# Kernel tuning notes

Measured on AMD Instinct MI355X. Metric: run time of the kernel, lower is better.

## Reference

```python
import jax, jax.numpy as jnp
import numpy as np
from jax import lax

B, T, H = 2, 1024, 2048
NH, D = 8, 128          # heads, head_dim
P = NH * D              # projection size
K = 4                   # short conv kernel size
EPS = 1e-6
SCALE = D ** -0.5


def _causal_conv_silu(x, w):
    # x: (B,T,C); w: (C,K) depthwise causal conv followed by silu (ShortConvolution)
    C = w.shape[0]
    kern = jnp.transpose(w)[:, None, :]  # (K,1,C)
    y = lax.conv_general_dilated(x, kern, window_strides=(1,), padding=[(K - 1, 0)],
                                 dimension_numbers=('NWC', 'WIO', 'NWC'),
                                 feature_group_count=C)
    return jax.nn.silu(y)


def _l2norm(x):
    return x * jax.lax.rsqrt(jnp.sum(x * x, axis=-1, keepdims=True) + EPS)


def _forward(hidden_states, Wq, Wk, Wv, conv_q, conv_k, conv_v, A_log, dt_bias,
             Wfa, Wfb, Wb, Wga, Wgb, norm_weight, Wo):
    x = hidden_states                                # (B,T,H)
    q = _causal_conv_silu(x @ Wq.T, conv_q)          # (B,T,P)
    k = _causal_conv_silu(x @ Wk.T, conv_k)
    v = _causal_conv_silu(x @ Wv.T, conv_v)
    # fused_kda_gate: g = -exp(A_log) * softplus(f_b(f_a(x)) + dt_bias), per (h,d) channel
    gf = (x @ Wfa.T) @ Wfb.T                         # (B,T,P) low-rank gate proj
    gf = gf.reshape(B, T, NH, D) + dt_bias.reshape(NH, D)
    g = -jnp.exp(A_log)[None, None, :, None] * jax.nn.softplus(gf)  # (B,T,NH,D) log-decay <= 0
    beta = jax.nn.sigmoid(x @ Wb.T)                  # (B,T,NH)
    q = _l2norm(q.reshape(B, T, NH, D)) * SCALE      # use_qk_l2norm_in_kernel + 1/sqrt(d) scale
    k = _l2norm(k.reshape(B, T, NH, D))
    v = v.reshape(B, T, NH, D)

    # gated delta-rule recurrence (KDA): per-key-channel decay, beta-weighted delta update
    def step(S, inp):
        q_t, k_t, v_t, g_t, b_t = inp                # (B,NH,D), beta (B,NH)
        S = S * jnp.exp(g_t)[..., None]              # decay rows (key dim) of S[.,.,dk,dv]
        kv = jnp.einsum('bhk,bhkv->bhv', k_t, S)
        delta = (v_t - kv) * b_t[..., None]
        S = S + jnp.einsum('bhk,bhv->bhkv', k_t, delta)
        o_t = jnp.einsum('bhk,bhkv->bhv', q_t, S)
        return S, o_t

    tfirst = lambda a: jnp.moveaxis(a, 1, 0)         # time-major for scan
    S0 = jnp.zeros((B, NH, D, D), x.dtype)
    _, o = lax.scan(step, S0, (tfirst(q), tfirst(k), tfirst(v), tfirst(g), tfirst(beta)))
    o = jnp.moveaxis(o, 0, 1)                        # (B,T,NH,D)

    # FusedRMSNormGated(sigmoid): gate applied before RMS normalization (Mamba2 convention)
    gate = ((x @ Wga.T) @ Wgb.T).reshape(B, T, NH, D)
    og = o * jax.nn.sigmoid(gate)
    og = og * jax.lax.rsqrt(jnp.mean(og * og, axis=-1, keepdims=True) + EPS) * norm_weight
    return og.reshape(B * T, P) @ Wo.T               # (B*T, H)


def setup_inputs():
    ks = jax.random.split(jax.random.key(0), 16)
    s = 0.02
    f32 = jnp.float32
    return {
        'hidden_states': jax.random.normal(ks[0], (B, T, H), f32),
        'Wq': jax.random.normal(ks[1], (P, H), f32) * s,
        'Wk': jax.random.normal(ks[2], (P, H), f32) * s,
        'Wv': jax.random.normal(ks[3], (P, H), f32) * s,
        'conv_q': jax.random.normal(ks[4], (P, K), f32) * 0.3,
        'conv_k': jax.random.normal(ks[5], (P, K), f32) * 0.3,
        'conv_v': jax.random.normal(ks[6], (P, K), f32) * 0.3,
        'A_log': jnp.log(jax.random.uniform(ks[7], (NH,), f32, 1.0, 16.0)),
        'dt_bias': jax.random.normal(ks[8], (P,), f32) * 0.5,
        'Wfa': jax.random.normal(ks[9], (D, H), f32) * s,
        'Wfb': jax.random.normal(ks[10], (P, D), f32) * s,
        'Wb': jax.random.normal(ks[11], (NH, H), f32) * s,
        'Wga': jax.random.normal(ks[12], (D, H), f32) * s,
        'Wgb': jax.random.normal(ks[13], (P, D), f32) * s,
        'norm_weight': jnp.ones((D,), f32),
        'Wo': jax.random.normal(ks[14], (H, P), f32) * s,
    }


def reference(hidden_states, Wq, Wk, Wv, conv_q, conv_k, conv_v, A_log, dt_bias,
              Wfa, Wfb, Wb, Wga, Wgb, norm_weight, Wo):
    return _forward(hidden_states, Wq, Wk, Wv, conv_q, conv_k, conv_v, A_log, dt_bias,
                    Wfa, Wfb, Wb, Wga, Wgb, norm_weight, Wo)
```

## Files before the change

kernel.cpp:

```cpp
#include <hip/hip_runtime.h>
#include <hip/hip_bf16.h>
#include <cstddef>
#include <cstdint>

#define Bb 2
#define Tt 1024
#define Hh 2048
#define NHh 8
#define Dd 128
#define Pp (NHh * Dd)
#define Kk 4
#define EPSf 1e-6f
#define SCALEf 0.08838834764831845f
#define DVQ 16
#define CHUNK 8

typedef short bf16x8 __attribute__((ext_vector_type(8)));
typedef float f32x4 __attribute__((ext_vector_type(4)));

template <int CTRL>
__device__ __forceinline__ float dpp_add(float x) {
  int yi = __builtin_amdgcn_update_dpp(0, __builtin_bit_cast(int, x), CTRL, 0xF, 0xF, true);
  return x + __builtin_bit_cast(float, yi);
}
__device__ __forceinline__ float row16_sum(float x) {
  x = dpp_add<0xB1>(x);
  x = dpp_add<0x4E>(x);
  x = dpp_add<0x124>(x);
  x = dpp_add<0x128>(x);
  return x;
}

__device__ __forceinline__ void gload_lds16(const void* g, void* l) {
  __builtin_amdgcn_global_load_lds((const __attribute__((address_space(1))) void*)g,
                                   (__attribute__((address_space(3))) void*)l, 16, 0, 0);
}

__global__ __launch_bounds__(256) void cvt_bf16(const float* __restrict__ src,
                                                __hip_bfloat16* __restrict__ dst, int n) {
  const int i = (blockIdx.x * 256 + threadIdx.x) * 8;
  if (i >= n) return;
  const float4 a = *reinterpret_cast<const float4*>(src + i);
  const float4 b = *reinterpret_cast<const float4*>(src + i + 4);
  __hip_bfloat16 t[8];
  t[0] = __float2bfloat16(a.x); t[1] = __float2bfloat16(a.y);
  t[2] = __float2bfloat16(a.z); t[3] = __float2bfloat16(a.w);
  t[4] = __float2bfloat16(b.x); t[5] = __float2bfloat16(b.y);
  t[6] = __float2bfloat16(b.z); t[7] = __float2bfloat16(b.w);
  *reinterpret_cast<uint4*>(dst + i) = *reinterpret_cast<const uint4*>(t);
}

__global__ __launch_bounds__(256) void cvt_bf16_x4(const float* __restrict__ s0,
                                                   const float* __restrict__ s1,
                                                   const float* __restrict__ s2,
                                                   const float* __restrict__ s3,
                                                   __hip_bfloat16* __restrict__ d0,
                                                   __hip_bfloat16* __restrict__ d1,
                                                   __hip_bfloat16* __restrict__ d2,
                                                   __hip_bfloat16* __restrict__ d3,
                                                   int nper) {
  const int bpa = nper / 2048;
  const int a = blockIdx.x / bpa;
  const int i = (blockIdx.x % bpa) * 2048 + threadIdx.x * 8;
  const float* src = (a == 0) ? s0 : (a == 1) ? s1 : (a == 2) ? s2 : s3;
  __hip_bfloat16* dst = (a == 0) ? d0 : (a == 1) ? d1 : (a == 2) ? d2 : d3;
  const float4 x = *reinterpret_cast<const float4*>(src + i);
  const float4 y = *reinterpret_cast<const float4*>(src + i + 4);
  __hip_bfloat16 t[8];
  t[0] = __float2bfloat16(x.x); t[1] = __float2bfloat16(x.y);
  t[2] = __float2bfloat16(x.z); t[3] = __float2bfloat16(x.w);
  t[4] = __float2bfloat16(y.x); t[5] = __float2bfloat16(y.y);
  t[6] = __float2bfloat16(y.z); t[7] = __float2bfloat16(y.w);
  *reinterpret_cast<uint4*>(dst + i) = *reinterpret_cast<const uint4*>(t);
}

__global__ __launch_bounds__(256) void cvt_split(const float* __restrict__ src,
                                                 __hip_bfloat16* __restrict__ hi,
                                                 __hip_bfloat16* __restrict__ lo, int n) {
  const int i = (blockIdx.x * 256 + threadIdx.x) * 8;
  if (i >= n) return;
  __hip_bfloat16 th[8], tl[8];
#pragma unroll
  for (int j = 0; j < 2; j++) {
    const float4 a = *reinterpret_cast<const float4*>(src + i + j * 4);
    const float f[4] = {a.x, a.y, a.z, a.w};
#pragma unroll
    for (int e = 0; e < 4; e++) {
      const __hip_bfloat16 h = __float2bfloat16(f[e]);
      th[j * 4 + e] = h;
      tl[j * 4 + e] = __float2bfloat16(f[e] - __bfloat162float(h));
    }
  }
  *reinterpret_cast<uint4*>(hi + i) = *reinterpret_cast<const uint4*>(th);
  *reinterpret_cast<uint4*>(lo + i) = *reinterpret_cast<const uint4*>(tl);
}

__global__ __launch_bounds__(256) void transpose_f32(const float* __restrict__ src,
                                                     float* __restrict__ dst, int R, int C) {
  __shared__ float t[32][33];
  const int bx = blockIdx.x * 32, by = blockIdx.y * 32;
  const int tx = threadIdx.x & 31, ty = threadIdx.x >> 5;
#pragma unroll
  for (int i = ty; i < 32; i += 8) {
    const int r = by + i, c = bx + tx;
    if (r < R && c < C) t[i][tx] = src[(size_t)r * C + c];
  }
  __syncthreads();
#pragma unroll
  for (int i = ty; i < 32; i += 8) {
    const int c = bx + i, r = by + tx;
    if (c < C && r < R) dst[(size_t)c * R + r] = t[tx][i];
  }
}

__global__ __launch_bounds__(256) void gemm_bf16_lds(const __hip_bfloat16* __restrict__ A,
                                                     const __hip_bfloat16* __restrict__ B,
                                                     float* __restrict__ C,
                                                     __hip_bfloat16* __restrict__ Cbf,
                                                     int M, int N, int K, int outmode) {
  __shared__ __align__(16) __hip_bfloat16 As[128 * 64];
  __shared__ __align__(16) __hip_bfloat16 Bs[128 * 64];
  const int tid = threadIdx.x;
  const int wave = tid >> 6;
  const int lane = tid & 63;
  const int wm = (wave >> 1) * 64;
  const int wn = (wave & 1) * 64;
  const int bm = blockIdx.y * 128;
  const int bn = blockIdx.x * 128;
  const int l15 = lane & 15;
  const int l4 = lane >> 4;
  const int srow = lane >> 3;
  const int scol = (lane & 7) * 8;

  f32x4 acc[4][4];
#pragma unroll
  for (int i = 0; i < 4; i++)
#pragma unroll
    for (int j = 0; j < 4; j++) acc[i][j] = (f32x4){0.f, 0.f, 0.f, 0.f};

  for (int k0 = 0; k0 < K; k0 += 64) {
#pragma unroll
    for (int i = 0; i < 4; i++) {
      const int s = wave * 4 + i;
      const int row = s * 8 + srow;
      gload_lds16(A + (size_t)(bm + row) * K + k0 + scol, &As[s * 512]);
      gload_lds16(B + (size_t)(bn + row) * K + k0 + scol, &Bs[s * 512]);
    }
    __syncthreads();
    bf16x8 af[4][2], bfv[4][2];
#pragma unroll
    for (int kf = 0; kf < 2; kf++) {
      const int kc = kf * 32 + l4 * 8;
#pragma unroll
      for (int mf = 0; mf < 4; mf++)
        af[mf][kf] = *reinterpret_cast<const bf16x8*>(&As[(wm + mf * 16 + l15) * 64 + kc]);
#pragma unroll
      for (int nf = 0; nf < 4; nf++)
        bfv[nf][kf] = *reinterpret_cast<const bf16x8*>(&Bs[(wn + nf * 16 + l15) * 64 + kc]);
    }
#pragma unroll
    for (int kf = 0; kf < 2; kf++)
#pragma unroll
      for (int mf = 0; mf < 4; mf++)
#pragma unroll
        for (int nf = 0; nf < 4; nf++)
          acc[mf][nf] = __builtin_amdgcn_mfma_f32_16x16x32_bf16(af[mf][kf], bfv[nf][kf],
                                                                acc[mf][nf], 0, 0, 0);
    __syncthreads();
  }
#pragma unroll
  for (int mf = 0; mf < 4; mf++) {
#pragma unroll
    for (int nf = 0; nf < 4; nf++) {
      const int col = bn + wn + nf * 16 + l15;
#pragma unroll
      for (int r = 0; r < 4; r++) {
        const int row = bm + wm + mf * 16 + l4 * 4 + r;
        if (outmode == 0) C[(size_t)row * N + col] = acc[mf][nf][r];
        else Cbf[(size_t)row * N + col] = __float2bfloat16(acc[mf][nf][r]);
      }
    }
  }
}

__global__ __launch_bounds__(256) void gemm_bf16_3t_lds(const __hip_bfloat16* __restrict__ Ahi,
                                                        const __hip_bfloat16* __restrict__ Alo,
                                                        const __hip_bfloat16* __restrict__ Bhi,
                                                        const __hip_bfloat16* __restrict__ Blo,
                                                        float* __restrict__ C,
                                                        int M, int N, int K) {
  __shared__ __align__(16) __hip_bfloat16 Ahs[64 * 64];
  __shared__ __align__(16) __hip_bfloat16 Als[64 * 64];
  __shared__ __align__(16) __hip_bfloat16 Bhs[128 * 64];
  __shared__ __align__(16) __hip_bfloat16 Bls[128 * 64];
  const int tid = threadIdx.x;
  const int wave = tid >> 6;
  const int lane = tid & 63;
  const int wm = (wave >> 1) * 32;
  const int wn = (wave & 1) * 64;
  const int bm = blockIdx.y * 64;
  const int bn = blockIdx.x * 128;
  const int l15 = lane & 15;
  const int l4 = lane >> 4;
  const int srow = lane >> 3;
  const int scol = (lane & 7) * 8;

  f32x4 acc[2][4];
#pragma unroll
  for (int i = 0; i < 2; i++)
#pragma unroll
    for (int j = 0; j < 4; j++) acc[i][j] = (f32x4){0.f, 0.f, 0.f, 0.f};

  for (int k0 = 0; k0 < K; k0 += 64) {
#pragma unroll
    for (int i = 0; i < 12; i++) {
      const int sid = wave * 12 + i;
      if (sid < 8) {
        const int row = sid * 8 + srow;
        gload_lds16(Ahi + (size_t)(bm + row) * K + k0 + scol, &Ahs[sid * 512]);
      } else if (sid < 16) {
        const int row = (sid - 8) * 8 + srow;
        gload_lds16(Alo + (size_t)(bm + row) * K + k0 + scol, &Als[(sid - 8) * 512]);
      } else if (sid < 32) {
        const int row = (sid - 16) * 8 + srow;
        gload_lds16(Bhi + (size_t)(bn + row) * K + k0 + scol, &Bhs[(sid - 16) * 512]);
      } else {
        const int row = (sid - 32) * 8 + srow;
        gload_lds16(Blo + (size_t)(bn + row) * K + k0 + scol, &Bls[(sid - 32) * 512]);
      }
    }
    __syncthreads();
#pragma unroll
    for (int kf = 0; kf < 2; kf++) {
      const int kc = kf * 32 + l4 * 8;
      bf16x8 ah[2], al[2], bh[4], bl[4];
#pragma unroll
      for (int mf = 0; mf < 2; mf++) {
        ah[mf] = *reinterpret_cast<const bf16x8*>(&Ahs[(wm + mf * 16 + l15) * 64 + kc]);
        al[mf] = *reinterpret_cast<const bf16x8*>(&Als[(wm + mf * 16 + l15) * 64 + kc]);
      }
#pragma unroll
      for (int nf = 0; nf < 4; nf++) {
        bh[nf] = *reinterpret_cast<const bf16x8*>(&Bhs[(wn + nf * 16 + l15) * 64 + kc]);
        bl[nf] = *reinterpret_cast<const bf16x8*>(&Bls[(wn + nf * 16 + l15) * 64 + kc]);
      }
#pragma unroll
      for (int mf = 0; mf < 2; mf++)
#pragma unroll
        for (int nf = 0; nf < 4; nf++) {
          acc[mf][nf] = __builtin_amdgcn_mfma_f32_16x16x32_bf16(ah[mf], bh[nf], acc[mf][nf], 0, 0, 0);
          acc[mf][nf] = __builtin_amdgcn_mfma_f32_16x16x32_bf16(ah[mf], bl[nf], acc[mf][nf], 0, 0, 0);
          acc[mf][nf] = __builtin_amdgcn_mfma_f32_16x16x32_bf16(al[mf], bh[nf], acc[mf][nf], 0, 0, 0);
        }
    }
    __syncthreads();
  }
#pragma unroll
  for (int mf = 0; mf < 2; mf++)
#pragma unroll
    for (int nf = 0; nf < 4; nf++) {
      const int col = bn + wn + nf * 16 + l15;
#pragma unroll
      for (int r = 0; r < 4; r++) {
        const int row = bm + wm + mf * 16 + l4 * 4 + r;
        C[(size_t)row * N + col] = acc[mf][nf][r];
      }
    }
}

__global__ __launch_bounds__(256) void gemm_nt(const float* __restrict__ A,
                                               const float* __restrict__ Bm,
                                               float* __restrict__ C,
                                               int M, int N, int Kd) {
  __shared__ float As[16][64];
  __shared__ float Bs[16][64];
  const int bm = blockIdx.y * 64;
  const int bn = blockIdx.x * 64;
  const int tid = threadIdx.x;
  const int tx = tid & 15;
  const int ty = tid >> 4;
  const int lr = tid >> 2;
  const int lc = (tid & 3) << 2;
  float acc[4][4];
#pragma unroll
  for (int i = 0; i < 4; i++)
#pragma unroll
    for (int j = 0; j < 4; j++) acc[i][j] = 0.f;
  for (int k0 = 0; k0 < Kd; k0 += 16) {
    float4 a4 = make_float4(0.f, 0.f, 0.f, 0.f);
    float4 b4 = make_float4(0.f, 0.f, 0.f, 0.f);
    const int ar = bm + lr;
    if (ar < M) a4 = *reinterpret_cast<const float4*>(A + (size_t)ar * Kd + k0 + lc);
    const int br = bn + lr;
    if (br < N) b4 = *reinterpret_cast<const float4*>(Bm + (size_t)br * Kd + k0 + lc);
    As[lc + 0][lr] = a4.x; As[lc + 1][lr] = a4.y; As[lc + 2][lr] = a4.z; As[lc + 3][lr] = a4.w;
    Bs[lc + 0][lr] = b4.x; Bs[lc + 1][lr] = b4.y; Bs[lc + 2][lr] = b4.z; Bs[lc + 3][lr] = b4.w;
    __syncthreads();
#pragma unroll
    for (int kk = 0; kk < 16; kk++) {
      float4 av = *reinterpret_cast<const float4*>(&As[kk][ty << 2]);
      float4 bv = *reinterpret_cast<const float4*>(&Bs[kk][tx << 2]);
      float a[4] = {av.x, av.y, av.z, av.w};
      float b[4] = {bv.x, bv.y, bv.z, bv.w};
#pragma unroll
      for (int i = 0; i < 4; i++)
#pragma unroll
        for (int j = 0; j < 4; j++) acc[i][j] += a[i] * b[j];
    }
    __syncthreads();
  }
#pragma unroll
  for (int i = 0; i < 4; i++) {
    const int row = bm + (ty << 2) + i;
    if (row >= M) continue;
#pragma unroll
    for (int j = 0; j < 4; j++) {
      const int col = bn + (tx << 2) + j;
      if (col < N) C[(size_t)row * N + col] = acc[i][j];
    }
  }
}

__global__ __launch_bounds__(256) void beta_kernel(const float* __restrict__ x,
                                                   const float* __restrict__ Wb,
                                                   float* __restrict__ beta) {
  __shared__ float xs[Hh];
  const int m = blockIdx.x;
  const int tid = threadIdx.x;
  for (int i = tid; i < Hh; i += 256) xs[i] = x[(size_t)m * Hh + i];
  __syncthreads();
  const int h = tid >> 5;
  const int lane = tid & 31;
  float acc = 0.f;
  for (int i = lane; i < Hh; i += 32) acc += xs[i] * Wb[(size_t)h * Hh + i];
#pragma unroll
  for (int o = 16; o > 0; o >>= 1) acc += __shfl_down(acc, o, 32);
  if (lane == 0) beta[(size_t)m * NHh + h] = 1.f / (1.f + expf(-acc));
}

__global__ __launch_bounds__(256) void g_kernel(float* __restrict__ gbuf,
                                                const float* __restrict__ dtb,
                                                const float* __restrict__ A_log) {
  const size_t i = (size_t)blockIdx.x * 256 + threadIdx.x;
  const int c = (int)(i % Pp);
  const int h = c / Dd;
  const float xv = gbuf[i] + dtb[c];
  const float sp = (xv > 20.f) ? xv : log1pf(expf(xv));
  gbuf[i] = expf(-expf(A_log[h]) * sp);
}

__global__ __launch_bounds__(128) void conv_silu_norm(const float* __restrict__ xin,
                                                      const float* __restrict__ w,
                                                      float* __restrict__ out,
                                                      int mode, int instride, int coff) {
  const int idx = blockIdx.x;
  const int h = idx % NHh;
  const int bt = idx / NHh;
  const int t = bt % Tt;
  const int d = threadIdx.x;
  const int c = h * Dd + d;
  float acc = 0.f;
#pragma unroll
  for (int j = 0; j < Kk; j++) {
    const int tt = t - (Kk - 1) + j;
    float xv = 0.f;
    if (tt >= 0) xv = xin[(size_t)(bt - (Kk - 1) + j) * instride + coff + c];
    acc += w[c * Kk + j] * xv;
  }
  float y = acc / (1.f + expf(-acc));
  float r = y;
  if (mode > 0) {
    float ss = y * y;
#pragma unroll
    for (int o = 32; o > 0; o >>= 1) ss += __shfl_down(ss, o);
    __shared__ float red[2];
    if ((d & 63) == 0) red[d >> 6] = ss;
    __syncthreads();
    const float tot = red[0] + red[1];
    const float inv = rsqrtf(tot + EPSf);
    r = y * inv * (mode == 2 ? SCALEf : 1.f);
  }
  out[(size_t)bt * Pp + c] = r;
}

__global__ __launch_bounds__(128) void scan_kernel(const float* __restrict__ q,
                                                   const float* __restrict__ k,
                                                   const float* __restrict__ v,
                                                   const float* __restrict__ eg,
                                                   const float* __restrict__ beta,
                                                   float* __restrict__ o) {
  const int blk = blockIdx.x;
  const int bh = blk & 15;
  const int dvq = blk >> 4;
  const int b = bh >> 3, h = bh & 7;
  const int tid = threadIdx.x;
  const int qr = tid & 15;
  const int dvl = tid >> 4;
  const int dv = dvq * 8 + dvl;

  __shared__ __align__(16) float qs[2][CHUNK][16][12];
  __shared__ __align__(16) float ks[2][CHUNK][16][12];
  __shared__ __align__(16) float legs[2][CHUNK][16][12];
  __shared__ float vs[2][CHUNK][8];
  __shared__ float betas[2][CHUNK];

  float s[8];
#pragma unroll
  for (int i = 0; i < 8; i++) s[i] = 0.f;

  const size_t base = (size_t)(b * Tt) * Pp + h * Dd;
  const int le = tid;

  float rq[CHUNK], rk[CHUNK], re[CHUNK], rv[CHUNK], rb = 0.f;
  auto load_chunk = [&](int t0) {
    const size_t coff = base + (size_t)t0 * Pp;
#pragma unroll
    for (int j = 0; j < CHUNK; j++) {
      rq[j] = q[coff + (size_t)j * Pp + le];
      rk[j] = k[coff + (size_t)j * Pp + le];
      re[j] = eg[coff + (size_t)j * Pp + le];
    }
    if (tid < 8) {
#pragma unroll
      for (int j = 0; j < CHUNK; j++) rv[j] = v[coff + (size_t)j * Pp + dvq * 8 + tid];
    } else if (tid < 8 + CHUNK) {
      rb = beta[(size_t)(b * Tt + t0 + tid - 8) * NHh + h];
    }
  };
  auto write_lds = [&](int bufw) {
#pragma unroll
    for (int j = 0; j < CHUNK; j++) {
      qs[bufw][j][le >> 3][le & 7] = rq[j];
      ks[bufw][j][le >> 3][le & 7] = rk[j];
      legs[bufw][j][le >> 3][le & 7] = re[j];
    }
    if (tid < 8) {
#pragma unroll
      for (int j = 0; j < CHUNK; j++) vs[bufw][j][tid] = rv[j];
    } else if (tid < 8 + CHUNK) {
      betas[bufw][tid - 8] = rb;
    }
  };

  load_chunk(0);
  write_lds(0);
  __syncthreads();
  const int NC = Tt / CHUNK;
  size_t off = base;
  for (int c = 0; c < NC; c++) {
    if (c + 1 < NC) load_chunk((c + 1) * CHUNK);
    const int buf = c & 1;
    float vv[CHUNK], bb[CHUNK], opart[CHUNK];
#pragma unroll
    for (int j = 0; j < CHUNK; j++) { vv[j] = vs[buf][j][dvl]; bb[j] = betas[buf][j]; }

    float4 ck0 = *reinterpret_cast<const float4*>(&ks[buf][0][qr][0]);
    float4 ck1 = *reinterpret_cast<const float4*>(&ks[buf][0][qr][4]);
    float4 ce0 = *reinterpret_cast<const float4*>(&legs[buf][0][qr][0]);
    float4 ce1 = *reinterpret_cast<const float4*>(&legs[buf][0][qr][4]);
    float4 cq0 = *reinterpret_cast<const float4*>(&qs[buf][0][qr][0]);
    float4 cq1 = *reinterpret_cast<const float4*>(&qs[buf][0][qr][4]);
    float kt0 = ck0.x * ce0.x, kt1 = ck0.y * ce0.y, kt2 = ck0.z * ce0.z, kt3 = ck0.w * ce0.w;
    float kt4 = ck1.x * ce1.x, kt5 = ck1.y * ce1.y, kt6 = ck1.z * ce1.z, kt7 = ck1.w * ce1.w;

#pragma unroll
    for (int j = 0; j < CHUNK; j++) {
      float4 nk0, nk1, ne0, ne1, nq0, nq1;
      if (j + 1 < CHUNK) {
        nk0 = *reinterpret_cast<const float4*>(&ks[buf][j + 1][qr][0]);
        nk1 = *reinterpret_cast<const float4*>(&ks[buf][j + 1][qr][4]);
        ne0 = *reinterpret_cast<const float4*>(&legs[buf][j + 1][qr][0]);
        ne1 = *reinterpret_cast<const float4*>(&legs[buf][j + 1][qr][4]);
        nq0 = *reinterpret_cast<const float4*>(&qs[buf][j + 1][qr][0]);
        nq1 = *reinterpret_cast<const float4*>(&qs[buf][j + 1][qr][4]);
      }
      const float es0 = ce0.x * s[0], es1 = ce0.y * s[1], es2 = ce0.z * s[2], es3 = ce0.w * s[3];
      const float es4 = ce1.x * s[4], es5 = ce1.y * s[5], es6 = ce1.z * s[6], es7 = ce1.w * s[7];
      float kva = kt0 * s[0] + kt4 * s[4];
      float kvb = kt1 * s[1] + kt5 * s[5];
      float kvc = kt2 * s[2] + kt6 * s[6];
      float kvd = kt3 * s[3] + kt7 * s[7];
      const float kvp = row16_sum((kva + kvb) + (kvc + kvd));
      const float delta = (vv[j] - kvp) * bb[j];
      s[0] = fmaf(ck0.x, delta, es0); float oa = cq0.x * s[0];
      s[1] = fmaf(ck0.y, delta, es1); float ob = cq0.y * s[1];
      s[2] = fmaf(ck0.z, delta, es2); float oc = cq0.z * s[2];
      s[3] = fmaf(ck0.w, delta, es3); float od = cq0.w * s[3];
      s[4] = fmaf(ck1.x, delta, es4); oa += cq1.x * s[4];
      s[5] = fmaf(ck1.y, delta, es5); ob += cq1.y * s[5];
      s[6] = fmaf(ck1.z, delta, es6); oc += cq1.z * s[6];
      s[7] = fmaf(ck1.w, delta, es7); od += cq1.w * s[7];
      opart[j] = (oa + ob) + (oc + od);
      if (j + 1 < CHUNK) {
        ck0 = nk0; ck1 = nk1; ce0 = ne0; ce1 = ne1; cq0 = nq0; cq1 = nq1;
        kt0 = ck0.x * ce0.x; kt1 = ck0.y * ce0.y; kt2 = ck0.z * ce0.z; kt3 = ck0.w * ce0.w;
        kt4 = ck1.x * ce1.x; kt5 = ck1.y * ce1.y; kt6 = ck1.z * ce1.z; kt7 = ck1.w * ce1.w;
      }
    }
#pragma unroll
    for (int j = 0; j < CHUNK; j++) opart[j] = row16_sum(opart[j]);
    if (qr == 0) {
#pragma unroll
      for (int j = 0; j < CHUNK; j++) o[off + (size_t)j * Pp + dv] = opart[j];
    }
    if (c + 1 < NC) write_lds(buf ^ 1);
    __syncthreads();
    off += (size_t)CHUNK * Pp;
  }
}

__global__ __launch_bounds__(128) void gated_norm(float* __restrict__ o,
                                                  const float* __restrict__ gate,
                                                  int gstride,
                                                  const float* __restrict__ nw,
                                                  __hip_bfloat16* __restrict__ ogbf) {
  const int idx = blockIdx.x;
  const int h = idx % NHh;
  const int bt = idx / NHh;
  const int d = threadIdx.x;
  const size_t off = (size_t)bt * Pp + h * Dd;
  const float ov = o[off + d];
  const float gt = gate[(size_t)bt * gstride + h * Dd + d];
  const float val = ov / (1.f + expf(-gt));
  float ss = val * val;
#pragma unroll
  for (int sh = 32; sh > 0; sh >>= 1) ss += __shfl_down(ss, sh);
  __shared__ float red[2];
  if ((d & 63) == 0) red[d >> 6] = ss;
  __syncthreads();
  const float mean = (red[0] + red[1]) * (1.f / Dd);
  const float res = val * rsqrtf(mean + EPSf) * nw[d];
  if (ogbf != nullptr) ogbf[off + d] = __float2bfloat16(res);
  else o[off + d] = res;
}

extern "C" void kernel_launch(void* const* d_in, const int* in_sizes, int n_in,
                              void* d_out, int out_size, void* d_ws, size_t ws_size,
                              hipStream_t stream) {
  const float* x     = (const float*)d_in[0];
  const float* Wq    = (const float*)d_in[1];
  const float* Wk    = (const float*)d_in[2];
  const float* Wv    = (const float*)d_in[3];
  const float* cq    = (const float*)d_in[4];
  const float* ck    = (const float*)d_in[5];
  const float* cv    = (const float*)d_in[6];
  const float* A_log = (const float*)d_in[7];
  const float* dtb   = (const float*)d_in[8];
  const float* Wfa   = (const float*)d_in[9];
  const float* Wfb   = (const float*)d_in[10];
  const float* Wb    = (const float*)d_in[11];
  const float* Wga   = (const float*)d_in[12];
  const float* Wgb   = (const float*)d_in[13];
  const float* nw    = (const float*)d_in[14];
  const float* Wo    = (const float*)d_in[15];
  float* outp = (float*)d_out;

  const int M = Bb * Tt;
  const size_t MP = (size_t)M * Pp;
  float* ws = (float*)d_ws;
  float* qkvpre = ws;
  float* qb   = qkvpre + 4 * MP;
  float* kb   = qb + MP;
  float* vb   = kb + MP;
  float* gbuf = vb + MP;
  float* obuf = gbuf + MP;
  float* betab = obuf + MP;
  float* WfaT = betab + (size_t)M * NHh;
  float* WgaT = WfaT + (size_t)Hh * Dd;
  float* f32end = WgaT + (size_t)Hh * Dd;
  float* Wcombf = obuf;

  __hip_bfloat16* xhi    = (__hip_bfloat16*)f32end;
  __hip_bfloat16* xlo    = xhi + (size_t)M * Hh;
  __hip_bfloat16* Wqkvbf = xlo + (size_t)M * Hh;
  __hip_bfloat16* Wobf   = Wqkvbf + (size_t)4 * Pp * Hh;
  __hip_bfloat16* WfaThi = Wobf + (size_t)Hh * Pp;
  __hip_bfloat16* WfaTlo = WfaThi + (size_t)Hh * Dd;
  __hip_bfloat16* Wfbhi  = WfaTlo + (size_t)Hh * Dd;
  __hip_bfloat16* Wfblo  = Wfbhi + (size_t)Pp * Dd;
  __hip_bfloat16* WgaTbf = Wfblo + (size_t)Pp * Dd;
  __hip_bfloat16* Wgbbf  = WgaTbf + (size_t)Hh * Dd;
  __hip_bfloat16* Wcombhi = Wgbbf + (size_t)Pp * Dd;
  __hip_bfloat16* Wcomblo = Wcombhi + (size_t)Pp * Hh;
  __hip_bfloat16* end = Wcomblo + (size_t)Pp * Hh;
  __hip_bfloat16* ogbf = xlo;
  const bool use_mfma = ws_size >= (size_t)((char*)end - (char*)d_ws);

  const dim3 blk(256);
  if (use_mfma) {
    cvt_split<<<(int)((size_t)M * Hh / 2048), blk, 0, stream>>>(x, xhi, xlo, M * Hh);
    cvt_bf16_x4<<<4 * (int)((size_t)Pp * Hh / 2048), blk, 0, stream>>>(
        Wq, Wk, Wv, Wo, Wqkvbf, Wqkvbf + (size_t)Pp * Hh, Wqkvbf + (size_t)2 * Pp * Hh,
        Wobf, Pp * Hh);
    transpose_f32<<<dim3(Hh / 32, Dd / 32), blk, 0, stream>>>(Wfa, WfaT, Dd, Hh);
    transpose_f32<<<dim3(Hh / 32, Dd / 32), blk, 0, stream>>>(Wga, WgaT, Dd, Hh);
    cvt_split<<<(int)((size_t)Hh * Dd / 2048), blk, 0, stream>>>(WfaT, WfaThi, WfaTlo, Hh * Dd);
    cvt_split<<<(int)((size_t)Pp * Dd / 2048), blk, 0, stream>>>(Wfb, Wfbhi, Wfblo, Pp * Dd);
    cvt_bf16<<<(int)((size_t)Hh * Dd / 2048), blk, 0, stream>>>(WgaT, WgaTbf, Hh * Dd);
    cvt_bf16<<<(int)((size_t)Pp * Dd / 2048), blk, 0, stream>>>(Wgb, Wgbbf, Pp * Dd);
    gemm_bf16_3t_lds<<<dim3(Hh / 128, Pp / 64), blk, 0, stream>>>(Wfbhi, Wfblo, WfaThi, WfaTlo,
                                                                  Wcombf, Pp, Hh, Dd);
    gemm_bf16_lds<<<dim3(Hh / 128, Pp / 128), blk, 0, stream>>>(Wgbbf, WgaTbf, nullptr,
                                                                Wqkvbf + (size_t)3 * Pp * Hh,
                                                                Pp, Hh, Dd, 1);
    cvt_split<<<(int)((size_t)Pp * Hh / 2048), blk, 0, stream>>>(Wcombf, Wcombhi, Wcomblo, Pp * Hh);
    gemm_bf16_lds<<<dim3(4 * Pp / 128, M / 128), blk, 0, stream>>>(xhi, Wqkvbf, qkvpre, nullptr,
                                                                   M, 4 * Pp, Hh, 0);
    gemm_bf16_3t_lds<<<dim3(Pp / 128, M / 64), blk, 0, stream>>>(xhi, xlo, Wcombhi, Wcomblo,
                                                                 gbuf, M, Pp, Hh);
    beta_kernel<<<M, 256, 0, stream>>>(x, Wb, betab);
    g_kernel<<<(int)(MP / 256), 256, 0, stream>>>(gbuf, dtb, A_log);
    conv_silu_norm<<<M * NHh, 128, 0, stream>>>(qkvpre, cq, qb, 2, 4 * Pp, 0);
    conv_silu_norm<<<M * NHh, 128, 0, stream>>>(qkvpre, ck, kb, 1, 4 * Pp, Pp);
    conv_silu_norm<<<M * NHh, 128, 0, stream>>>(qkvpre, cv, vb, 0, 4 * Pp, 2 * Pp);
    scan_kernel<<<Bb * NHh * DVQ, 128, 0, stream>>>(qb, kb, vb, gbuf, betab, obuf);
    gated_norm<<<M * NHh, 128, 0, stream>>>(obuf, qkvpre + (size_t)3 * Pp, 4 * Pp, nw, ogbf);
    gemm_bf16_lds<<<dim3(Hh / 128, M / 128), blk, 0, stream>>>(ogbf, Wobf, outp, nullptr, M, Hh, Pp, 0);
  } else {
    float* qpre = qkvpre;
    float* kpre = qkvpre + MP;
    float* vpre = qkvpre + 2 * MP;
    float* gate = qkvpre + 3 * MP;
    float* gfa = WfaT;
    float* gga = WgaT;
    gemm_nt<<<dim3(Pp / 64, M / 64), blk, 0, stream>>>(x, Wq, qpre, M, Pp, Hh);
    gemm_nt<<<dim3(Pp / 64, M / 64), blk, 0, stream>>>(x, Wk, kpre, M, Pp, Hh);
    gemm_nt<<<dim3(Pp / 64, M / 64), blk, 0, stream>>>(x, Wv, vpre, M, Pp, Hh);
    gemm_nt<<<dim3(Dd / 64, M / 64), blk, 0, stream>>>(x, Wfa, gfa, M, Dd, Hh);
    gemm_nt<<<dim3(Dd / 64, M / 64), blk, 0, stream>>>(x, Wga, gga, M, Dd, Hh);
    gemm_nt<<<dim3(Pp / 64, M / 64), blk, 0, stream>>>(gfa, Wfb, gbuf, M, Pp, Dd);
    gemm_nt<<<dim3(Pp / 64, M / 64), blk, 0, stream>>>(gga, Wgb, gate, M, Pp, Dd);
    beta_kernel<<<M, 256, 0, stream>>>(x, Wb, betab);
    g_kernel<<<(int)(MP / 256), 256, 0, stream>>>(gbuf, dtb, A_log);
    conv_silu_norm<<<M * NHh, 128, 0, stream>>>(qpre, cq, qb, 2, Pp, 0);
    conv_silu_norm<<<M * NHh, 128, 0, stream>>>(kpre, ck, kb, 1, Pp, 0);
    conv_silu_norm<<<M * NHh, 128, 0, stream>>>(vpre, cv, vb, 0, Pp, 0);
    scan_kernel<<<Bb * NHh * DVQ, 128, 0, stream>>>(qb, kb, vb, gbuf, betab, obuf);
    gated_norm<<<M * NHh, 128, 0, stream>>>(obuf, gate, Pp, nw, nullptr);
    gemm_nt<<<dim3(Hh / 64, M / 64), blk, 0, stream>>>(obuf, Wo, outp, M, Hh, Pp);
  }
}
```

Baseline: 470.3 us.

## Fuse gate activation into GEMM epilogue, merge conv launches, pack scan math

Moves the softplus/exp decay computation into the epilogue of the gate GEMM, so the separate g_kernel pass over gbuf goes away. The three conv_silu_norm launches become a single conv3_kernel launch that writes q, k and v into consecutive buffers, which assumes qb, kb and vb are laid out contiguously. The scan inner loop is rewritten with two-wide float vectors so the compiler can emit packed FP32 instructions. The aim is to cut kernel launches and memory passes and to raise ALU throughput on the serial scan.

Result: faster. 456.7 us (-2.9%).

```diff
diff --git a/kernel.cpp b/kernel.cpp
--- a/kernel.cpp
+++ b/kernel.cpp
@@ -17,6 +17,7 @@
 
 typedef short bf16x8 __attribute__((ext_vector_type(8)));
 typedef float f32x4 __attribute__((ext_vector_type(4)));
+typedef float f32x2 __attribute__((ext_vector_type(2)));
 
 template <int CTRL>
 __device__ __forceinline__ float dpp_add(float x) {
@@ -188,7 +189,10 @@
                                                         const __hip_bfloat16* __restrict__ Bhi,
                                                         const __hip_bfloat16* __restrict__ Blo,
                                                         float* __restrict__ C,
-                                                        int M, int N, int K) {
+                                                        int M, int N, int K,
+                                                        const float* __restrict__ dtb,
+                                                        const float* __restrict__ A_log,
+                                                        int gmode) {
   __shared__ __align__(16) __hip_bfloat16 Ahs[64 * 64];
   __shared__ __align__(16) __hip_bfloat16 Als[64 * 64];
   __shared__ __align__(16) __hip_bfloat16 Bhs[128 * 64];
@@ -263,7 +267,13 @@
 #pragma unroll
       for (int r = 0; r < 4; r++) {
         const int row = bm + wm + mf * 16 + l4 * 4 + r;
-        C[(size_t)row * N + col] = acc[mf][nf][r];
+        float val = acc[mf][nf][r];
+        if (gmode) {
+          const float xv = val + dtb[col];
+          const float sp = (xv > 20.f) ? xv : log1pf(expf(xv));
+          val = expf(-expf(A_log[col >> 7]) * sp);
+        }
+        C[(size_t)row * N + col] = val;
       }
     }
 }
@@ -383,6 +393,45 @@
   out[(size_t)bt * Pp + c] = r;
 }
 
+__global__ __launch_bounds__(128) void conv3_kernel(const float* __restrict__ qkvpre,
+                                                    const float* __restrict__ cq,
+                                                    const float* __restrict__ ck,
+                                                    const float* __restrict__ cv,
+                                                    float* __restrict__ outbase) {
+  const int nblk = Bb * Tt * NHh;
+  const int which = blockIdx.x / nblk;
+  const int idx = blockIdx.x % nblk;
+  const float* w = (which == 0) ? cq : (which == 1) ? ck : cv;
+  const int mode = (which == 0) ? 2 : (which == 1) ? 1 : 0;
+  const int h = idx % NHh;
+  const int bt = idx / NHh;
+  const int t = bt % Tt;
+  const int d = threadIdx.x;
+  const int c = h * Dd + d;
+  float acc = 0.f;
+#pragma unroll
+  for (int j = 0; j < Kk; j++) {
+    const int tt = t - (Kk - 1) + j;
+    float xv = 0.f;
+    if (tt >= 0) xv = qkvpre[(size_t)(bt - (Kk - 1) + j) * (4 * Pp) + which * Pp + c];
+    acc += w[c * Kk + j] * xv;
+  }
+  float y = acc / (1.f + expf(-acc));
+  float r = y;
+  if (mode > 0) {
+    float ss = y * y;
+#pragma unroll
+    for (int o = 32; o > 0; o >>= 1) ss += __shfl_down(ss, o);
+    __shared__ float red[2];
+    if ((d & 63) == 0) red[d >> 6] = ss;
+    __syncthreads();
+    const float tot = red[0] + red[1];
+    const float inv = rsqrtf(tot + EPSf);
+    r = y * inv * (mode == 2 ? SCALEf : 1.f);
+  }
+  outbase[(size_t)which * (Bb * Tt) * Pp + (size_t)bt * Pp + c] = r;
+}
+
 __global__ __launch_bounds__(128) void scan_kernel(const float* __restrict__ q,
                                                    const float* __restrict__ k,
                                                    const float* __restrict__ v,
@@ -404,9 +453,9 @@
   __shared__ float vs[2][CHUNK][8];
   __shared__ float betas[2][CHUNK];
 
-  float s[8];
-#pragma unroll
-  for (int i = 0; i < 8; i++) s[i] = 0.f;
+  f32x2 s2[4];
+#pragma unroll
+  for (int i = 0; i < 4; i++) s2[i] = (f32x2){0.f, 0.f};
 
   const size_t base = (size_t)(b * Tt) * Pp + h * Dd;
   const int le = tid;
@@ -440,6 +489,10 @@
     } else if (tid < 8 + CHUNK) {
       betas[bufw][tid - 8] = rb;
     }
+  };
+  auto unpack = [](const float4& a, const float4& b, f32x2 out[4]) {
+    out[0] = (f32x2){a.x, a.y}; out[1] = (f32x2){a.z, a.w};
+    out[2] = (f32x2){b.x, b.y}; out[3] = (f32x2){b.z, b.w};
   };
 
   load_chunk(0);
@@ -454,14 +507,18 @@
 #pragma unroll
     for (int j = 0; j < CHUNK; j++) { vv[j] = vs[buf][j][dvl]; bb[j] = betas[buf][j]; }
 
-    float4 ck0 = *reinterpret_cast<const float4*>(&ks[buf][0][qr][0]);
-    float4 ck1 = *reinterpret_cast<const float4*>(&ks[buf][0][qr][4]);
-    float4 ce0 = *reinterpret_cast<const float4*>(&legs[buf][0][qr][0]);
-    float4 ce1 = *reinterpret_cast<const float4*>(&legs[buf][0][qr][4]);
-    float4 cq0 = *reinterpret_cast<const float4*>(&qs[buf][0][qr][0]);
-    float4 cq1 = *reinterpret_cast<const float4*>(&qs[buf][0][qr][4]);
-    float kt0 = ck0.x * ce0.x, kt1 = ck0.y * ce0.y, kt2 = ck0.z * ce0.z, kt3 = ck0.w * ce0.w;
-    float kt4 = ck1.x * ce1.x, kt5 = ck1.y * ce1.y, kt6 = ck1.z * ce1.z, kt7 = ck1.w * ce1.w;
+    f32x2 ck2[4], ce2[4], cq2[4], kt2[4];
+    {
+      const float4 k0 = *reinterpret_cast<const float4*>(&ks[buf][0][qr][0]);
+      const float4 k1 = *reinterpret_cast<const float4*>(&ks[buf][0][qr][4]);
+      const float4 e0 = *reinterpret_cast<const float4*>(&legs[buf][0][qr][0]);
+      const float4 e1 = *reinterpret_cast<const float4*>(&legs[buf][0][qr][4]);
+      const float4 q0 = *reinterpret_cast<const float4*>(&qs[buf][0][qr][0]);
+      const float4 q1 = *reinterpret_cast<const float4*>(&qs[buf][0][qr][4]);
+      unpack(k0, k1, ck2); unpack(e0, e1, ce2); unpack(q0, q1, cq2);
+#pragma unroll
+      for (int i = 0; i < 4; i++) kt2[i] = ck2[i] * ce2[i];
+    }
 
 #pragma unroll
     for (int j = 0; j < CHUNK; j++) {
@@ -474,27 +531,26 @@
         nq0 = *reinterpret_cast<const float4*>(&qs[buf][j + 1][qr][0]);
         nq1 = *reinterpret_cast<const float4*>(&qs[buf][j + 1][qr][4]);
       }
-      const float es0 = ce0.x * s[0], es1 = ce0.y * s[1], es2 = ce0.z * s[2], es3 = ce0.w * s[3];
-      const float es4 = ce1.x * s[4], es5 = ce1.y * s[5], es6 = ce1.z * s[6], es7 = ce1.w * s[7];
-      float kva = kt0 * s[0] + kt4 * s[4];
-      float kvb = kt1 * s[1] + kt5 * s[5];
-      float kvc = kt2 * s[2] + kt6 * s[6];
-      float kvd = kt3 * s[3] + kt7 * s[7];
-      const float kvp = row16_sum((kva + kvb) + (kvc + kvd));
+      f32x2 es0 = ce2[0] * s2[0], es1 = ce2[1] * s2[1];
+      f32x2 es2v = ce2[2] * s2[2], es3 = ce2[3] * s2[3];
+      f32x2 kva = kt2[0] * s2[0];
+      f32x2 kvb = kt2[1] * s2[1];
+      kva = kt2[2] * s2[2] + kva;
+      kvb = kt2[3] * s2[3] + kvb;
+      kva = kva + kvb;
+      const float kvp = row16_sum(kva.x + kva.y);
       const float delta = (vv[j] - kvp) * bb[j];
-      s[0] = fmaf(ck0.x, delta, es0); float oa = cq0.x * s[0];
-      s[1] = fmaf(ck0.y, delta, es1); float ob = cq0.y * s[1];
-      s[2] = fmaf(ck0.z, delta, es2); float oc = cq0.z * s[2];
-      s[3] = fmaf(ck0.w, delta, es3); float od = cq0.w * s[3];
-      s[4] = fmaf(ck1.x, delta, es4); oa += cq1.x * s[4];
-      s[5] = fmaf(ck1.y, delta, es5); ob += cq1.y * s[5];
-      s[6] = fmaf(ck1.z, delta, es6); oc += cq1.z * s[6];
-      s[7] = fmaf(ck1.w, delta, es7); od += cq1.w * s[7];
-      opart[j] = (oa + ob) + (oc + od);
+      const f32x2 d2 = (f32x2){delta, delta};
+      f32x2 o2;
+      s2[0] = ck2[0] * d2 + es0;  o2 = cq2[0] * s2[0];
+      s2[1] = ck2[1] * d2 + es1;  o2 = cq2[1] * s2[1] + o2;
+      s2[2] = ck2[2] * d2 + es2v; o2 = cq2[2] * s2[2] + o2;
+      s2[3] = ck2[3] * d2 + es3;  o2 = cq2[3] * s2[3] + o2;
+      opart[j] = o2.x + o2.y;
       if (j + 1 < CHUNK) {
-        ck0 = nk0; ck1 = nk1; ce0 = ne0; ce1 = ne1; cq0 = nq0; cq1 = nq1;
-        kt0 = ck0.x * ce0.x; kt1 = ck0.y * ce0.y; kt2 = ck0.z * ce0.z; kt3 = ck0.w * ce0.w;
-        kt4 = ck1.x * ce1.x; kt5 = ck1.y * ce1.y; kt6 = ck1.z * ce1.z; kt7 = ck1.w * ce1.w;
+        unpack(nk0, nk1, ck2); unpack(ne0, ne1, ce2); unpack(nq0, nq1, cq2);
+#pragma unroll
+        for (int i = 0; i < 4; i++) kt2[i] = ck2[i] * ce2[i];
       }
     }
 #pragma unroll
@@ -599,7 +655,8 @@
     cvt_bf16<<<(int)((size_t)Hh * Dd / 2048), blk, 0, stream>>>(WgaT, WgaTbf, Hh * Dd);
     cvt_bf16<<<(int)((size_t)Pp * Dd / 2048), blk, 0, stream>>>(Wgb, Wgbbf, Pp * Dd);
     gemm_bf16_3t_lds<<<dim3(Hh / 128, Pp / 64), blk, 0, stream>>>(Wfbhi, Wfblo, WfaThi, WfaTlo,
-                                                                  Wcombf, Pp, Hh, Dd);
+                                                                  Wcombf, Pp, Hh, Dd,
+                                                                  nullptr, nullptr, 0);
     gemm_bf16_lds<<<dim3(Hh / 128, Pp / 128), blk, 0, stream>>>(Wgbbf, WgaTbf, nullptr,
                                                                 Wqkvbf + (size_t)3 * Pp * Hh,
                                                                 Pp, Hh, Dd, 1);
@@ -607,12 +664,10 @@
     gemm_bf16_lds<<<dim3(4 * Pp / 128, M / 128), blk, 0, stream>>>(xhi, Wqkvbf, qkvpre, nullptr,
                                                                    M, 4 * Pp, Hh, 0);
     gemm_bf16_3t_lds<<<dim3(Pp / 128, M / 64), blk, 0, stream>>>(xhi, xlo, Wcombhi, Wcomblo,
-                                                                 gbuf, M, Pp, Hh);
+                                                                 gbuf, M, Pp, Hh,
+                                                                 dtb, A_log, 1);
     beta_kernel<<<M, 256, 0, stream>>>(x, Wb, betab);
-    g_kernel<<<(int)(MP / 256), 256, 0, stream>>>(gbuf, dtb, A_log);
-    conv_silu_norm<<<M * NHh, 128, 0, stream>>>(qkvpre, cq, qb, 2, 4 * Pp, 0);
-    conv_silu_norm<<<M * NHh, 128, 0, stream>>>(qkvpre, ck, kb, 1, 4 * Pp, Pp);
-    conv_silu_norm<<<M * NHh, 128, 0, stream>>>(qkvpre, cv, vb, 0, 4 * Pp, 2 * Pp);
+    conv3_kernel<<<3 * M * NHh, 128, 0, stream>>>(qkvpre, cq, ck, cv, qb);
     scan_kernel<<<Bb * NHh * DVQ, 128, 0, stream>>>(qb, kb, vb, gbuf, betab, obuf);
     gated_norm<<<M * NHh, 128, 0, stream>>>(obuf, qkvpre + (size_t)3 * Pp, 4 * Pp, nw, ogbf);
     gemm_bf16_lds<<<dim3(Hh / 128, M / 128), blk, 0, stream>>>(ogbf, Wobf, outp, nullptr, M, Hh, Pp, 0);
```
